# Performance work log

Measured on AMD Instinct MI355X. Metric: run time of the kernel, lower is better.

Reference implementation:

```python
import jax, jax.numpy as jnp
import numpy as np

N_NODES = 50000
N_EDGES = 400000
D_IN = 256
D_OUT = 256
DROPOUT_P = 0.1


def setup_inputs() -> dict:
    key = jax.random.key(0)
    k_feat, k_w, k_src, k_dst = jax.random.split(key, 4)
    feat = jax.random.normal(k_feat, (N_NODES, D_IN), dtype=jnp.float32)
    # Glorot-ish init for the GraphConv weight
    W = jax.random.normal(k_w, (D_IN, D_OUT), dtype=jnp.float32) * (1.0 / np.sqrt(D_IN))
    b = jnp.zeros((D_OUT,), dtype=jnp.float32)
    src = jax.random.randint(k_src, (N_EDGES,), 0, N_NODES, dtype=jnp.int32)
    dst = jax.random.randint(k_dst, (N_EDGES,), 0, N_NODES, dtype=jnp.int32)
    return {"feat": feat, "W": W, "b": b, "src": src, "dst": dst}


def reference(feat, W, b, src, dst):
    # Degrees from the edge list (DGL GraphConv norm='both'):
    # src is normalized by out-degree, dst by in-degree; clamp to >= 1.
    ones = jnp.ones((src.shape[0],), dtype=feat.dtype)
    deg_out = jnp.clip(jax.ops.segment_sum(ones, src, num_segments=N_NODES), 1.0)
    deg_in = jnp.clip(jax.ops.segment_sum(ones, dst, num_segments=N_NODES), 1.0)

    # Pre-normalize, project, then gather-scatter aggregate (mult W first,
    # mathematically identical to DGL's ordering since dims are equal).
    x = feat * jax.lax.rsqrt(deg_out)[:, None]          # [N, D_in]
    x = x @ W                                            # [N, D_out]
    agg = jax.ops.segment_sum(x[src], dst, num_segments=N_NODES)  # [N, D_out]
    h = agg * jax.lax.rsqrt(deg_in)[:, None] + b

    # Activation + dropout (training-mode, deterministic key)
    h = jax.nn.relu(h)
    keep = jax.random.bernoulli(jax.random.key(42), 1.0 - DROPOUT_P, h.shape)
    h = jnp.where(keep, h / (1.0 - DROPOUT_P), 0.0)
    return h
```

## Files before the change

### kernel.cpp

```cpp
#include <hip/hip_runtime.h>
#include <stdint.h>

#define N_NODES 50000
#define N_EDGES 400000
#define DDIM 256
#define MASK_WORDS 400000
#define EDGE_CAP 64
#define FCONV_BLOCKS 6250
#define FILL_BLOCKS 391
#define MASK_BLOCKS 1563

typedef __attribute__((ext_vector_type(8))) short bf16x8;
typedef __attribute__((ext_vector_type(4))) float f32x4;

__device__ __forceinline__ uint32_t rotl32(uint32_t x, uint32_t r) {
  return (x << r) | (x >> (32u - r));
}

__device__ __forceinline__ uint32_t threefry_draw_0_42(uint32_t x0, uint32_t x1) {
  const uint32_t k0 = 0u, k1 = 42u;
  const uint32_t k2 = k0 ^ k1 ^ 0x1BD11BDAu;
  x0 += k0;
  x1 += k1;
#define TF_ROUND(r)          \
  {                          \
    x0 += x1;                \
    x1 = rotl32(x1, r);      \
    x1 ^= x0;                \
  }
  TF_ROUND(13) TF_ROUND(15) TF_ROUND(26) TF_ROUND(6)
  x0 += k1; x1 += k2 + 1u;
  TF_ROUND(17) TF_ROUND(29) TF_ROUND(16) TF_ROUND(24)
  x0 += k2; x1 += k0 + 2u;
  TF_ROUND(13) TF_ROUND(15) TF_ROUND(26) TF_ROUND(6)
  x0 += k0; x1 += k1 + 3u;
  TF_ROUND(17) TF_ROUND(29) TF_ROUND(16) TF_ROUND(24)
  x0 += k1; x1 += k2 + 4u;
  TF_ROUND(13) TF_ROUND(15) TF_ROUND(26) TF_ROUND(6)
  x0 += k2; x1 += k0 + 5u;
#undef TF_ROUND
  return x0 ^ x1;
}

__device__ __forceinline__ uint16_t bf16_rne(float x) {
  uint32_t u = __float_as_uint(x);
  u += 0x7FFFu + ((u >> 16) & 1u);
  return (uint16_t)(u >> 16);
}

__global__ __launch_bounds__(256) void setup_kernel(
    const float* __restrict__ W, uint16_t* __restrict__ Wt,
    int4* __restrict__ zero_base) {
  const int bid = blockIdx.x;
  if (bid < 98) {
    const int t = bid * 256 + threadIdx.x;
    if (t < 25000) zero_base[t] = make_int4(0, 0, 0, 0);
  } else {
    const int t = (bid - 98) * 256 + threadIdx.x;
    const int n = t >> 6;
    const int k4 = (t & 63) << 2;
    ushort4 p;
    p.x = bf16_rne(W[(size_t)(k4 + 0) * DDIM + n]);
    p.y = bf16_rne(W[(size_t)(k4 + 1) * DDIM + n]);
    p.z = bf16_rne(W[(size_t)(k4 + 2) * DDIM + n]);
    p.w = bf16_rne(W[(size_t)(k4 + 3) * DDIM + n]);
    *(ushort4*)(Wt + (size_t)n * DDIM + k4) = p;
  }
}

__global__ __launch_bounds__(256) void deghist_kernel(
    const int* __restrict__ src, int* __restrict__ deg_out) {
  const int base = (blockIdx.x * 256 + threadIdx.x) * 4;
  if (base < N_EDGES) {
    const int4 s = *(const int4*)(src + base);
    atomicAdd(&deg_out[s.x], 1);
    atomicAdd(&deg_out[s.y], 1);
    atomicAdd(&deg_out[s.z], 1);
    atomicAdd(&deg_out[s.w], 1);
  }
}

__global__ __launch_bounds__(256) void fused_prep_kernel(
    const float* __restrict__ feat, const int* __restrict__ src,
    const int* __restrict__ dst, const int* __restrict__ deg_out,
    int* __restrict__ deg_in, int* __restrict__ esrc,
    uint32_t* __restrict__ mask, uint16_t* __restrict__ featb) {
  const int bid = blockIdx.x;
  if (bid < FCONV_BLOCKS) {
    const int t = bid * 256 + threadIdx.x;
    const size_t base = (size_t)t * 8;
    const int row = t >> 5;
    const float sc = rsqrtf(fmaxf((float)deg_out[row], 1.0f));
    const float4 a = *(const float4*)(feat + base);
    const float4 b = *(const float4*)(feat + base + 4);
    ushort4 lo, hi;
    lo.x = bf16_rne(a.x * sc); lo.y = bf16_rne(a.y * sc);
    lo.z = bf16_rne(a.z * sc); lo.w = bf16_rne(a.w * sc);
    hi.x = bf16_rne(b.x * sc); hi.y = bf16_rne(b.y * sc);
    hi.z = bf16_rne(b.z * sc); hi.w = bf16_rne(b.w * sc);
    *(ushort4*)(featb + base) = lo;
    *(ushort4*)(featb + base + 4) = hi;
  } else if (bid < FCONV_BLOCKS + FILL_BLOCKS) {
    const int base = ((bid - FCONV_BLOCKS) * 256 + threadIdx.x) * 4;
    if (base < N_EDGES) {
      const int4 s4 = *(const int4*)(src + base);
      const int4 d4 = *(const int4*)(dst + base);
      const int p0 = atomicAdd(&deg_in[d4.x], 1);
      const int p1 = atomicAdd(&deg_in[d4.y], 1);
      const int p2 = atomicAdd(&deg_in[d4.z], 1);
      const int p3 = atomicAdd(&deg_in[d4.w], 1);
      if (p0 < EDGE_CAP) esrc[(d4.x << 6) + p0] = s4.x;
      if (p1 < EDGE_CAP) esrc[(d4.y << 6) + p1] = s4.y;
      if (p2 < EDGE_CAP) esrc[(d4.z << 6) + p2] = s4.z;
      if (p3 < EDGE_CAP) esrc[(d4.w << 6) + p3] = s4.w;
    }
  } else {
    const uint32_t t =
        (uint32_t)(bid - FCONV_BLOCKS - FILL_BLOCKS) * 256u + (uint32_t)threadIdx.x;
    if (t < MASK_WORDS) {
      const uint32_t base = t * 32u;
      uint32_t w = 0u;
#pragma unroll
      for (uint32_t b = 0; b < 32u; ++b) {
        const uint32_t bits = threefry_draw_0_42(0u, base + b);
        w |= ((bits >> 9) < 7549747u) ? (1u << b) : 0u;
      }
      mask[t] = w;
    }
  }
}

__device__ __forceinline__ void acc8(float* a, uint4 q) {
  a[0] += __uint_as_float(q.x << 16);
  a[1] += __uint_as_float(q.x & 0xFFFF0000u);
  a[2] += __uint_as_float(q.y << 16);
  a[3] += __uint_as_float(q.y & 0xFFFF0000u);
  a[4] += __uint_as_float(q.z << 16);
  a[5] += __uint_as_float(q.z & 0xFFFF0000u);
  a[6] += __uint_as_float(q.w << 16);
  a[7] += __uint_as_float(q.w & 0xFFFF0000u);
}

__global__ __launch_bounds__(256) void gather_kernel(
    const uint16_t* __restrict__ featb, const int* __restrict__ deg_in,
    const int* __restrict__ esrc, uint16_t* __restrict__ agg) {
  const int n = blockIdx.x * 8 + (threadIdx.x >> 5);
  if (n >= N_NODES) return;
  const int l32 = threadIdx.x & 31;
  const size_t coff = (size_t)(l32 << 3);
  const int beg = n << 6;
  const int cnt = min(deg_in[n], EDGE_CAP);

  float a[8] = {};
  int j = 0;
  for (; j + 8 <= cnt; j += 8) {
    const int4 e0 = *(const int4*)(esrc + beg + j);
    const int4 e1 = *(const int4*)(esrc + beg + j + 4);
    const uint4 q0 = *(const uint4*)(featb + (size_t)e0.x * DDIM + coff);
    const uint4 q1 = *(const uint4*)(featb + (size_t)e0.y * DDIM + coff);
    const uint4 q2 = *(const uint4*)(featb + (size_t)e0.z * DDIM + coff);
    const uint4 q3 = *(const uint4*)(featb + (size_t)e0.w * DDIM + coff);
    const uint4 q4 = *(const uint4*)(featb + (size_t)e1.x * DDIM + coff);
    const uint4 q5 = *(const uint4*)(featb + (size_t)e1.y * DDIM + coff);
    const uint4 q6 = *(const uint4*)(featb + (size_t)e1.z * DDIM + coff);
    const uint4 q7 = *(const uint4*)(featb + (size_t)e1.w * DDIM + coff);
    acc8(a, q0); acc8(a, q1); acc8(a, q2); acc8(a, q3);
    acc8(a, q4); acc8(a, q5); acc8(a, q6); acc8(a, q7);
  }
  if (j + 4 <= cnt) {
    const int4 e0 = *(const int4*)(esrc + beg + j);
    const uint4 q0 = *(const uint4*)(featb + (size_t)e0.x * DDIM + coff);
    const uint4 q1 = *(const uint4*)(featb + (size_t)e0.y * DDIM + coff);
    const uint4 q2 = *(const uint4*)(featb + (size_t)e0.z * DDIM + coff);
    const uint4 q3 = *(const uint4*)(featb + (size_t)e0.w * DDIM + coff);
    acc8(a, q0); acc8(a, q1); acc8(a, q2); acc8(a, q3);
    j += 4;
  }
  if (j + 2 <= cnt) {
    const int s0 = esrc[beg + j];
    const int s1 = esrc[beg + j + 1];
    const uint4 q0 = *(const uint4*)(featb + (size_t)s0 * DDIM + coff);
    const uint4 q1 = *(const uint4*)(featb + (size_t)s1 * DDIM + coff);
    acc8(a, q0); acc8(a, q1);
    j += 2;
  }
  if (j < cnt) {
    const int s0 = esrc[beg + j];
    const uint4 q0 = *(const uint4*)(featb + (size_t)s0 * DDIM + coff);
    acc8(a, q0);
  }

  uint4 p;
  p.x = (uint32_t)bf16_rne(a[0]) | ((uint32_t)bf16_rne(a[1]) << 16);
  p.y = (uint32_t)bf16_rne(a[2]) | ((uint32_t)bf16_rne(a[3]) << 16);
  p.z = (uint32_t)bf16_rne(a[4]) | ((uint32_t)bf16_rne(a[5]) << 16);
  p.w = (uint32_t)bf16_rne(a[6]) | ((uint32_t)bf16_rne(a[7]) << 16);
  *(uint4*)(agg + (size_t)n * DDIM + coff) = p;
}

#define APAD 280
__global__ __launch_bounds__(256, 4) void gemm_mfma_kernel(
    const uint16_t* __restrict__ agg, const uint16_t* __restrict__ Wt,
    const float* __restrict__ bias, const int* __restrict__ deg_in,
    const uint32_t* __restrict__ mask, float* __restrict__ out) {
  __shared__ short As[64 * APAD];
  __shared__ float sdeg[64];
  __shared__ float sbias[256];

  const int tid = threadIdx.x;
  const int r0 = blockIdx.x * 64;
  const int lane = tid & 63;
  const int seg = lane >> 4;
  const int l15 = lane & 15;
  const int wc = tid >> 6;

  sbias[tid] = bias[tid];
  if (tid < 64) {
    const int r = r0 + tid;
    sdeg[tid] = (r < N_NODES) ? rsqrtf(fmaxf((float)deg_in[r], 1.0f)) : 0.0f;
  }

  {
    const uint16_t* ap = agg + (size_t)r0 * DDIM;
#pragma unroll
    for (int it = 0; it < 8; ++it) {
      const int c = tid + 256 * it;
      const int row = c >> 5;
      const int k8 = (c & 31) << 3;
      int4 v = make_int4(0, 0, 0, 0);
      if (r0 + row < N_NODES) v = *(const int4*)(ap + (size_t)row * DDIM + k8);
      *(int4*)&As[row * APAD + k8] = v;
    }
  }
  __syncthreads();

  const uint16_t* wt_base = Wt + (size_t)(wc * 64 + l15) * DDIM + seg * 8;

  f32x4 acc[4][4] = {};
#pragma unroll
  for (int kkI = 0; kkI < 8; ++kkI) {
    const int kk = kkI * 32;
    bf16x8 a[4], b[4];
#pragma unroll
    for (int m = 0; m < 4; ++m)
      a[m] = *(const bf16x8*)&As[(m * 16 + l15) * APAD + kk + seg * 8];
#pragma unroll
    for (int n = 0; n < 4; ++n)
      b[n] = *(const bf16x8*)(wt_base + n * 16 * DDIM + kk);
#pragma unroll
    for (int m = 0; m < 4; ++m)
#pragma unroll
      for (int n = 0; n < 4; ++n)
        acc[m][n] = __builtin_amdgcn_mfma_f32_16x16x32_bf16(a[m], b[n], acc[m][n], 0, 0, 0);
  }

  constexpr float INV09 = 1.0f / 0.9f;
#pragma unroll
  for (int m = 0; m < 4; ++m) {
#pragma unroll
    for (int r = 0; r < 4; ++r) {
      const int lrow = m * 16 + seg * 4 + r;
      const int row = r0 + lrow;
      if (row >= N_NODES) continue;
      const float s = sdeg[lrow];
      const uint32_t w0 = mask[row * 8 + wc * 2];
      const uint32_t w1 = mask[row * 8 + wc * 2 + 1];
#pragma unroll
      for (int n = 0; n < 4; ++n) {
        const int col = wc * 64 + n * 16 + l15;
        float v = fmaxf(acc[m][n][r] * s + sbias[col], 0.0f);
        const uint32_t w = (n < 2) ? w0 : w1;
        const uint32_t bit = (uint32_t)((n & 1) * 16 + l15);
        out[(size_t)row * DDIM + col] = ((w >> bit) & 1u) ? v * INV09 : 0.0f;
      }
    }
  }
}

extern "C" void kernel_launch(void* const* d_in, const int* in_sizes, int n_in,
                              void* d_out, int out_size, void* d_ws, size_t ws_size,
                              hipStream_t stream) {
  const float* feat = (const float*)d_in[0];
  const float* W = (const float*)d_in[1];
  const float* bias = (const float*)d_in[2];
  const int* src = (const int*)d_in[3];
  const int* dst = (const int*)d_in[4];
  float* out = (float*)d_out;

  char* ws = (char*)d_ws;
  int* deg_out = (int*)(ws + 0);
  int* deg_in = (int*)(ws + 200000);
  int* esrc = (int*)(ws + 400000);
  uint16_t* Wt = (uint16_t*)(ws + 13200000);
  uint16_t* featb = (uint16_t*)(ws + 13331072);
  uint32_t* mask = (uint32_t*)(ws + 38931072);
  uint16_t* agg = (uint16_t*)(ws + 40531072);

  setup_kernel<<<162, 256, 0, stream>>>(W, Wt, (int4*)d_ws);
  deghist_kernel<<<391, 256, 0, stream>>>(src, deg_out);
  fused_prep_kernel<<<FCONV_BLOCKS + FILL_BLOCKS + MASK_BLOCKS, 256, 0, stream>>>(
      feat, src, dst, deg_out, deg_in, esrc, mask, featb);
  gather_kernel<<<(N_NODES + 7) / 8, 256, 0, stream>>>(featb, deg_in, esrc, agg);
  gemm_mfma_kernel<<<(N_NODES + 63) / 64, 256, 0, stream>>>(agg, Wt, bias, deg_in, mask, out);
}
```

Baseline: 129.7 us.

## Move out-degree scaling into gather and merge degree histogram into prep kernel

The feature conversion no longer scales by rsqrt(out-degree). Each source row's scale is now applied in the gather kernel, read per edge from deg_out. Because nothing in the prep step depends on deg_out any more, the separate degree-histogram kernel is folded into the edge-fill branch of one prep kernel, saving a launch and a serialization point. The cost is an extra scattered deg_out load plus an rsqrt per edge, and fma accumulation in the gather. Rounding also changes slightly, since unscaled features are now rounded to bf16.

```diff
diff --git a/kernel.cpp b/kernel.cpp
--- a/kernel.cpp
+++ b/kernel.cpp
@@ -6,9 +6,9 @@
 #define DDIM 256
 #define MASK_WORDS 400000
 #define EDGE_CAP 64
+#define EDGE_BLOCKS 391
+#define MASK_BLOCKS 1563
 #define FCONV_BLOCKS 6250
-#define FILL_BLOCKS 391
-#define MASK_BLOCKS 1563
 
 typedef __attribute__((ext_vector_type(8))) short bf16x8;
 typedef __attribute__((ext_vector_type(4))) float f32x4;
@@ -68,43 +68,21 @@
   }
 }
 
-__global__ __launch_bounds__(256) void deghist_kernel(
-    const int* __restrict__ src, int* __restrict__ deg_out) {
-  const int base = (blockIdx.x * 256 + threadIdx.x) * 4;
-  if (base < N_EDGES) {
-    const int4 s = *(const int4*)(src + base);
-    atomicAdd(&deg_out[s.x], 1);
-    atomicAdd(&deg_out[s.y], 1);
-    atomicAdd(&deg_out[s.z], 1);
-    atomicAdd(&deg_out[s.w], 1);
-  }
-}
-
-__global__ __launch_bounds__(256) void fused_prep_kernel(
+__global__ __launch_bounds__(256) void mega_prep_kernel(
     const float* __restrict__ feat, const int* __restrict__ src,
-    const int* __restrict__ dst, const int* __restrict__ deg_out,
+    const int* __restrict__ dst, int* __restrict__ deg_out,
     int* __restrict__ deg_in, int* __restrict__ esrc,
     uint32_t* __restrict__ mask, uint16_t* __restrict__ featb) {
   const int bid = blockIdx.x;
-  if (bid < FCONV_BLOCKS) {
-    const int t = bid * 256 + threadIdx.x;
-    const size_t base = (size_t)t * 8;
-    const int row = t >> 5;
-    const float sc = rsqrtf(fmaxf((float)deg_out[row], 1.0f));
-    const float4 a = *(const float4*)(feat + base);
-    const float4 b = *(const float4*)(feat + base + 4);
-    ushort4 lo, hi;
-    lo.x = bf16_rne(a.x * sc); lo.y = bf16_rne(a.y * sc);
-    lo.z = bf16_rne(a.z * sc); lo.w = bf16_rne(a.w * sc);
-    hi.x = bf16_rne(b.x * sc); hi.y = bf16_rne(b.y * sc);
-    hi.z = bf16_rne(b.z * sc); hi.w = bf16_rne(b.w * sc);
-    *(ushort4*)(featb + base) = lo;
-    *(ushort4*)(featb + base + 4) = hi;
-  } else if (bid < FCONV_BLOCKS + FILL_BLOCKS) {
-    const int base = ((bid - FCONV_BLOCKS) * 256 + threadIdx.x) * 4;
+  if (bid < EDGE_BLOCKS) {
+    const int base = (bid * 256 + threadIdx.x) * 4;
     if (base < N_EDGES) {
       const int4 s4 = *(const int4*)(src + base);
       const int4 d4 = *(const int4*)(dst + base);
+      atomicAdd(&deg_out[s4.x], 1);
+      atomicAdd(&deg_out[s4.y], 1);
+      atomicAdd(&deg_out[s4.z], 1);
+      atomicAdd(&deg_out[s4.w], 1);
       const int p0 = atomicAdd(&deg_in[d4.x], 1);
       const int p1 = atomicAdd(&deg_in[d4.y], 1);
       const int p2 = atomicAdd(&deg_in[d4.z], 1);
@@ -114,9 +92,9 @@
       if (p2 < EDGE_CAP) esrc[(d4.z << 6) + p2] = s4.z;
       if (p3 < EDGE_CAP) esrc[(d4.w << 6) + p3] = s4.w;
     }
-  } else {
+  } else if (bid < EDGE_BLOCKS + MASK_BLOCKS) {
     const uint32_t t =
-        (uint32_t)(bid - FCONV_BLOCKS - FILL_BLOCKS) * 256u + (uint32_t)threadIdx.x;
+        (uint32_t)(bid - EDGE_BLOCKS) * 256u + (uint32_t)threadIdx.x;
     if (t < MASK_WORDS) {
       const uint32_t base = t * 32u;
       uint32_t w = 0u;
@@ -127,23 +105,40 @@
       }
       mask[t] = w;
     }
-  }
-}
-
-__device__ __forceinline__ void acc8(float* a, uint4 q) {
-  a[0] += __uint_as_float(q.x << 16);
-  a[1] += __uint_as_float(q.x & 0xFFFF0000u);
-  a[2] += __uint_as_float(q.y << 16);
-  a[3] += __uint_as_float(q.y & 0xFFFF0000u);
-  a[4] += __uint_as_float(q.z << 16);
-  a[5] += __uint_as_float(q.z & 0xFFFF0000u);
-  a[6] += __uint_as_float(q.w << 16);
-  a[7] += __uint_as_float(q.w & 0xFFFF0000u);
+  } else {
+    const int t = (bid - EDGE_BLOCKS - MASK_BLOCKS) * 256 + threadIdx.x;
+    const size_t base = (size_t)t * 8;
+    const float4 a = *(const float4*)(feat + base);
+    const float4 b = *(const float4*)(feat + base + 4);
+    ushort4 lo, hi;
+    lo.x = bf16_rne(a.x); lo.y = bf16_rne(a.y);
+    lo.z = bf16_rne(a.z); lo.w = bf16_rne(a.w);
+    hi.x = bf16_rne(b.x); hi.y = bf16_rne(b.y);
+    hi.z = bf16_rne(b.z); hi.w = bf16_rne(b.w);
+    *(ushort4*)(featb + base) = lo;
+    *(ushort4*)(featb + base + 4) = hi;
+  }
+}
+
+__device__ __forceinline__ void acc8s(float* a, uint4 q, float sc) {
+  a[0] = fmaf(__uint_as_float(q.x << 16), sc, a[0]);
+  a[1] = fmaf(__uint_as_float(q.x & 0xFFFF0000u), sc, a[1]);
+  a[2] = fmaf(__uint_as_float(q.y << 16), sc, a[2]);
+  a[3] = fmaf(__uint_as_float(q.y & 0xFFFF0000u), sc, a[3]);
+  a[4] = fmaf(__uint_as_float(q.z << 16), sc, a[4]);
+  a[5] = fmaf(__uint_as_float(q.z & 0xFFFF0000u), sc, a[5]);
+  a[6] = fmaf(__uint_as_float(q.w << 16), sc, a[6]);
+  a[7] = fmaf(__uint_as_float(q.w & 0xFFFF0000u), sc, a[7]);
+}
+
+__device__ __forceinline__ float dscale(const int* deg, int s) {
+  return rsqrtf(fmaxf((float)deg[s], 1.0f));
 }
 
 __global__ __launch_bounds__(256) void gather_kernel(
-    const uint16_t* __restrict__ featb, const int* __restrict__ deg_in,
-    const int* __restrict__ esrc, uint16_t* __restrict__ agg) {
+    const uint16_t* __restrict__ featb, const int* __restrict__ deg_out,
+    const int* __restrict__ deg_in, const int* __restrict__ esrc,
+    uint16_t* __restrict__ agg) {
   const int n = blockIdx.x * 8 + (threadIdx.x >> 5);
   if (n >= N_NODES) return;
   const int l32 = threadIdx.x & 31;
@@ -164,8 +159,16 @@
     const uint4 q5 = *(const uint4*)(featb + (size_t)e1.y * DDIM + coff);
     const uint4 q6 = *(const uint4*)(featb + (size_t)e1.z * DDIM + coff);
     const uint4 q7 = *(const uint4*)(featb + (size_t)e1.w * DDIM + coff);
-    acc8(a, q0); acc8(a, q1); acc8(a, q2); acc8(a, q3);
-    acc8(a, q4); acc8(a, q5); acc8(a, q6); acc8(a, q7);
+    const float s0 = dscale(deg_out, e0.x);
+    const float s1 = dscale(deg_out, e0.y);
+    const float s2 = dscale(deg_out, e0.z);
+    const float s3 = dscale(deg_out, e0.w);
+    const float s4 = dscale(deg_out, e1.x);
+    const float s5 = dscale(deg_out, e1.y);
+    const float s6 = dscale(deg_out, e1.z);
+    const float s7 = dscale(deg_out, e1.w);
+    acc8s(a, q0, s0); acc8s(a, q1, s1); acc8s(a, q2, s2); acc8s(a, q3, s3);
+    acc8s(a, q4, s4); acc8s(a, q5, s5); acc8s(a, q6, s6); acc8s(a, q7, s7);
   }
   if (j + 4 <= cnt) {
     const int4 e0 = *(const int4*)(esrc + beg + j);
@@ -173,21 +176,26 @@
     const uint4 q1 = *(const uint4*)(featb + (size_t)e0.y * DDIM + coff);
     const uint4 q2 = *(const uint4*)(featb + (size_t)e0.z * DDIM + coff);
     const uint4 q3 = *(const uint4*)(featb + (size_t)e0.w * DDIM + coff);
-    acc8(a, q0); acc8(a, q1); acc8(a, q2); acc8(a, q3);
+    const float s0 = dscale(deg_out, e0.x);
+    const float s1 = dscale(deg_out, e0.y);
+    const float s2 = dscale(deg_out, e0.z);
+    const float s3 = dscale(deg_out, e0.w);
+    acc8s(a, q0, s0); acc8s(a, q1, s1); acc8s(a, q2, s2); acc8s(a, q3, s3);
     j += 4;
   }
   if (j + 2 <= cnt) {
-    const int s0 = esrc[beg + j];
-    const int s1 = esrc[beg + j + 1];
-    const uint4 q0 = *(const uint4*)(featb + (size_t)s0 * DDIM + coff);
-    const uint4 q1 = *(const uint4*)(featb + (size_t)s1 * DDIM + coff);
-    acc8(a, q0); acc8(a, q1);
+    const int s0i = esrc[beg + j];
+    const int s1i = esrc[beg + j + 1];
+    const uint4 q0 = *(const uint4*)(featb + (size_t)s0i * DDIM + coff);
+    const uint4 q1 = *(const uint4*)(featb + (size_t)s1i * DDIM + coff);
+    acc8s(a, q0, dscale(deg_out, s0i));
+    acc8s(a, q1, dscale(deg_out, s1i));
     j += 2;
   }
   if (j < cnt) {
-    const int s0 = esrc[beg + j];
-    const uint4 q0 = *(const uint4*)(featb + (size_t)s0 * DDIM + coff);
-    acc8(a, q0);
+    const int s0i = esrc[beg + j];
+    const uint4 q0 = *(const uint4*)(featb + (size_t)s0i * DDIM + coff);
+    acc8s(a, q0, dscale(deg_out, s0i));
   }
 
   uint4 p;
@@ -297,9 +305,8 @@
   uint16_t* agg = (uint16_t*)(ws + 40531072);
 
   setup_kernel<<<162, 256, 0, stream>>>(W, Wt, (int4*)d_ws);
-  deghist_kernel<<<391, 256, 0, stream>>>(src, deg_out);
-  fused_prep_kernel<<<FCONV_BLOCKS + FILL_BLOCKS + MASK_BLOCKS, 256, 0, stream>>>(
+  mega_prep_kernel<<<EDGE_BLOCKS + MASK_BLOCKS + FCONV_BLOCKS, 256, 0, stream>>>(
       feat, src, dst, deg_out, deg_in, esrc, mask, featb);
-  gather_kernel<<<(N_NODES + 7) / 8, 256, 0, stream>>>(featb, deg_in, esrc, agg);
+  gather_kernel<<<(N_NODES + 7) / 8, 256, 0, stream>>>(featb, deg_out, deg_in, esrc, agg);
   gemm_mfma_kernel<<<(N_NODES + 63) / 64, 256, 0, stream>>>(agg, Wt, bias, deg_in, mask, out);
 }
```

Measured after the change: 117.5 us. 9.4% less time.
